# Performance work log

Hardware: AMD Instinct MI355X
Metric: run time of the kernel (lower is better)

The kernel has to match this reference:

```python
import jax, jax.numpy as jnp
import numpy as np

# Attention(d_model=1024, d_head=64, h=16, fastmax=True) -> fastmax_custom path with
# mask=True, normalize=True, temperature=1, a0=1, a1=1, lim=1, p=1, zero RPE.
B, N, D_MODEL, H, D_HEAD = 1, 2048, 1024, 16, 64
A0, A1, LIM = 1.0, 1.0, 1.0


def setup_inputs() -> dict:
    key = jax.random.key(0)
    ks = jax.random.split(key, 6)
    s = 1.0 / np.sqrt(D_MODEL).astype(np.float32)
    return {
        "X": jax.random.normal(ks[0], (B, N, D_MODEL), jnp.float32),
        "Wq": jax.random.normal(ks[1], (H * D_HEAD, D_MODEL), jnp.float32) * s,
        "Wk": jax.random.normal(ks[2], (H * D_HEAD, D_MODEL), jnp.float32) * s,
        "Wv": jax.random.normal(ks[3], (H * D_HEAD, D_MODEL), jnp.float32) * s,
        "Wo": jax.random.normal(ks[4], (D_MODEL, H * D_HEAD), jnp.float32) * s,
        "bo": jnp.zeros((D_MODEL,), jnp.float32),
    }


def _fastmax_causal_p1(q, k, v):
    # q,k,v: [b,h,n,d]. fastmax normalize: scale q,k so the max per-token L2 norm
    # (over the sequence, per batch-head) equals LIM; temperature forced to 1.
    qn = jnp.max(jnp.linalg.norm(q, axis=-1), axis=-1)[..., None, None]  # [b,h,1,1]
    kn = jnp.max(jnp.linalg.norm(k, axis=-1), axis=-1)[..., None, None]
    q = LIM * q / qn
    k = LIM * k / kn
    n = q.shape[2]
    # first-order (p=1) polynomial kernel attention, causal via prefix sums:
    #   score(i,j) = a0 + a1 * <q_i, k_j>,  j <= i
    kv = jnp.cumsum(k[..., :, None] * v[..., None, :], axis=2)  # [b,h,n,d,d]
    num = A0 * jnp.cumsum(v, axis=2) + A1 * jnp.einsum('bhnd,bhnde->bhne', q, kv)
    ksum = jnp.cumsum(k, axis=2)  # [b,h,n,d]
    den = A0 * jnp.arange(1, n + 1, dtype=q.dtype) + A1 * jnp.einsum('bhnd,bhnd->bhn', q, ksum)
    return num / den[..., None]


def reference(X, Wq, Wk, Wv, Wo, bo):
    b, n, _ = X.shape

    def heads(W):
        # [b,n,d_model] @ [d_model,h*d] -> [b,h,n,d]
        return (X @ W.T).reshape(b, n, H, D_HEAD).transpose(0, 2, 1, 3)

    q, k, v = heads(Wq), heads(Wk), heads(Wv)
    vh = _fastmax_causal_p1(q, k, v)                       # [b,h,n,d]
    vh = vh.transpose(0, 2, 1, 3).reshape(b, n, H * D_HEAD)
    return vh @ Wo.T + bo                                  # eval mode: dropout is identity
```

## Files before the change

### kernel.cpp

```cpp
#include <hip/hip_runtime.h>

#define N_SEQ 2048
#define NH 16
#define DH 64
#define CHUNK 64
#define NCHUNK 32

typedef float f32x4 __attribute__((ext_vector_type(4)));
typedef __bf16 bf16x8 __attribute__((ext_vector_type(8)));
typedef unsigned short u16x4 __attribute__((ext_vector_type(4)));
typedef unsigned short u16x8 __attribute__((ext_vector_type(8)));

static __device__ inline unsigned short f2b(float x) {
    unsigned int u = __builtin_bit_cast(unsigned int, x);
    unsigned int r = (u + 0x7fffu + ((u >> 16) & 1u)) >> 16;
    return (unsigned short)r;
}
static __device__ inline float b2f(unsigned short b) {
    return __builtin_bit_cast(float, (unsigned int)b << 16);
}
static __device__ inline int sw(int row, int col) {
    return row * 64 + (col ^ ((row & 7) << 3));
}

__global__ __launch_bounds__(256) void cast_all(
    const float* __restrict__ X, const float* __restrict__ Wq, const float* __restrict__ Wk,
    const float* __restrict__ Wv, const float* __restrict__ Wo,
    unsigned short* __restrict__ Xb, unsigned short* __restrict__ Wb,
    unsigned short* __restrict__ Wob) {
    int i = blockIdx.x * 256 + threadIdx.x;
    const float* src; unsigned short* dst; int off;
    if (i < 524288)       { src = X;  dst = Xb;               off = i; }
    else if (i < 786432)  { src = Wq; dst = Wb;               off = i - 524288; }
    else if (i < 1048576) { src = Wk; dst = Wb + (1u << 20);  off = i - 786432; }
    else if (i < 1310720) { src = Wv; dst = Wb + (2u << 20);  off = i - 1048576; }
    else                  { src = Wo; dst = Wob;              off = i - 1310720; }
    float4 v = reinterpret_cast<const float4*>(src)[off];
    u16x4 o;
    o[0] = f2b(v.x); o[1] = f2b(v.y); o[2] = f2b(v.z); o[3] = f2b(v.w);
    reinterpret_cast<u16x4*>(dst)[off] = o;
}

static __device__ inline void gload_lds16(const unsigned short* g, unsigned short* l) {
    __builtin_amdgcn_global_load_lds(
        (const __attribute__((address_space(1))) unsigned int*)g,
        (__attribute__((address_space(3))) unsigned int*)l, 16, 0, 0);
}

template<int MODE, int BM>
__global__ __launch_bounds__(256, 2) void gemm_bf16(
    const unsigned short* __restrict__ A,
    const unsigned short* __restrict__ B,
    float* __restrict__ outf,
    unsigned short* __restrict__ outb,
    const float* __restrict__ bias,
    int M, int N, int K)
{
    __shared__ __align__(16) unsigned short As[BM][32];
    __shared__ __align__(16) unsigned short Bs[128][32];

    const int L = blockIdx.y * gridDim.x + blockIdx.x;
    const int cpx = (gridDim.x * gridDim.y) >> 3;
    const int tile = (L & 7) * cpx + (L >> 3);
    const int bn = tile / gridDim.y;
    const int bm = tile % gridDim.y;

    const int t = threadIdx.x;
    const int wave = t >> 6, lane = t & 63;
    const int wm = wave >> 1, wn = wave & 1;
    const int r16 = lane & 15, ks = lane >> 4;
    constexpr int MFRAG = BM / 32;

    f32x4 acc[MFRAG][4] = {};

    const unsigned short* gA = A + (size_t)bm * BM * K;
    const unsigned short* gB = B + (size_t)bn * 128 * K;
    const int lrow = lane >> 2;
    const int lcol = (lane & 3) * 8;

    for (int k0 = 0; k0 < K; k0 += 32) {
        __syncthreads();
        #pragma unroll
        for (int p = 0; p < BM / 64; ++p) {
            int row = p * 64 + wave * 16;
            gload_lds16(&gA[(size_t)(row + lrow) * K + k0 + lcol], &As[row][0]);
        }
        #pragma unroll
        for (int p = 0; p < 2; ++p) {
            int row = p * 64 + wave * 16;
            gload_lds16(&gB[(size_t)(row + lrow) * K + k0 + lcol], &Bs[row][0]);
        }
        __syncthreads();

        bf16x8 af[MFRAG], bfr[4];
        #pragma unroll
        for (int m = 0; m < MFRAG; ++m)
            af[m] = *reinterpret_cast<const bf16x8*>(&As[wm * (BM / 2) + m * 16 + r16][ks * 8]);
        #pragma unroll
        for (int n = 0; n < 4; ++n)
            bfr[n] = *reinterpret_cast<const bf16x8*>(&Bs[wn * 64 + n * 16 + r16][ks * 8]);
        #pragma unroll
        for (int m = 0; m < MFRAG; ++m)
            #pragma unroll
            for (int n = 0; n < 4; ++n)
                acc[m][n] = __builtin_amdgcn_mfma_f32_16x16x32_bf16(af[m], bfr[n], acc[m][n], 0, 0, 0);
    }

    #pragma unroll
    for (int m = 0; m < MFRAG; ++m) {
        int row0 = bm * BM + wm * (BM / 2) + m * 16 + ks * 4;
        #pragma unroll
        for (int n = 0; n < 4; ++n) {
            int col = bn * 128 + wn * 64 + n * 16 + r16;
            if (MODE == 0) {
                int wch = col >> 10, h = (col >> 6) & 15, d = col & 63;
                unsigned short* dst = outb + (size_t)wch * (NH * (size_t)N_SEQ * DH)
                                          + (size_t)h * N_SEQ * DH + d;
                #pragma unroll
                for (int j = 0; j < 4; ++j)
                    dst[(size_t)(row0 + j) * DH] = f2b(acc[m][n][j]);
            } else {
                float bv = bias[col];
                #pragma unroll
                for (int j = 0; j < 4; ++j)
                    outf[(size_t)(row0 + j) * N + col] = acc[m][n][j] + bv;
            }
        }
    }
}

__global__ __launch_bounds__(256) void norms1(const unsigned short* __restrict__ QK,
                                              float* __restrict__ partial) {
    const int b = blockIdx.x;
    const int rc = b & 7, h = (b >> 3) & 15, which = b >> 7;
    const int t = threadIdx.x;
    const unsigned short* base = QK + ((size_t)(which * 16 + h) * N_SEQ + rc * 256 + t) * DH;
    float s = 0.f;
    #pragma unroll
    for (int i = 0; i < 8; ++i) {
        u16x8 v = *reinterpret_cast<const u16x8*>(base + i * 8);
        #pragma unroll
        for (int j = 0; j < 8; ++j) { float f = b2f(v[j]); s += f * f; }
    }
    #pragma unroll
    for (int off = 1; off < 64; off <<= 1) s = fmaxf(s, __shfl_xor(s, off));
    __shared__ float red[4];
    if ((t & 63) == 0) red[t >> 6] = s;
    __syncthreads();
    if (t == 0) partial[b] = fmaxf(fmaxf(red[0], red[1]), fmaxf(red[2], red[3]));
}

__global__ __launch_bounds__(256) void chunk_sums(const unsigned short* __restrict__ Kb,
                                                  const unsigned short* __restrict__ Vb,
                                                  unsigned short* __restrict__ Ssum,
                                                  float* __restrict__ zsum,
                                                  float* __restrict__ vssum) {
    const int h = blockIdx.x >> 5, c = blockIdx.x & 31;
    __shared__ __align__(16) unsigned short Kt[4096];
    __shared__ __align__(16) unsigned short Vt[4096];
    const size_t off = ((size_t)h * N_SEQ + c * CHUNK) * DH;
    const int t = threadIdx.x, lane = t & 63;

    {
        const int d = t & 63, j0 = (t >> 6) * 16;
        unsigned short rk[16], rv[16];
        #pragma unroll
        for (int i = 0; i < 16; ++i) {
            rk[i] = Kb[off + (size_t)(j0 + i) * DH + d];
            rv[i] = Vb[off + (size_t)(j0 + i) * DH + d];
        }
        u16x8 a, b;
        #pragma unroll
        for (int i = 0; i < 8; ++i) { a[i] = rk[i]; b[i] = rk[8 + i]; }
        *reinterpret_cast<u16x8*>(&Kt[sw(d, j0)]) = a;
        *reinterpret_cast<u16x8*>(&Kt[sw(d, j0 + 8)]) = b;
        #pragma unroll
        for (int i = 0; i < 8; ++i) { a[i] = rv[i]; b[i] = rv[8 + i]; }
        *reinterpret_cast<u16x8*>(&Vt[sw(d, j0)]) = a;
        *reinterpret_cast<u16x8*>(&Vt[sw(d, j0 + 8)]) = b;
    }
    __syncthreads();

    const int w = t >> 6, cl = lane & 15, g = lane >> 4;
    bf16x8 ak0 = *reinterpret_cast<const bf16x8*>(&Kt[sw(w * 16 + cl, g * 8)]);
    bf16x8 ak1 = *reinterpret_cast<const bf16x8*>(&Kt[sw(w * 16 + cl, 32 + g * 8)]);
    f32x4 acc[4] = {};
    #pragma unroll
    for (int et = 0; et < 4; ++et) {
        bf16x8 b0 = *reinterpret_cast<const bf16x8*>(&Vt[sw(et * 16 + cl, g * 8)]);
        bf16x8 b1 = *reinterpret_cast<const bf16x8*>(&Vt[sw(et * 16 + cl, 32 + g * 8)]);
        acc[et] = __builtin_amdgcn_mfma_f32_16x16x32_bf16(ak0, b0, acc[et], 0, 0, 0);
        acc[et] = __builtin_amdgcn_mfma_f32_16x16x32_bf16(ak1, b1, acc[et], 0, 0, 0);
    }
    unsigned short* So = Ssum + (size_t)blockIdx.x * (DH * DH);
    #pragma unroll
    for (int et = 0; et < 4; ++et)
        #pragma unroll
        for (int j = 0; j < 4; ++j)
            So[(size_t)(w * 16 + g * 4 + j) * DH + et * 16 + cl] = f2b(acc[et][j]);

    if (t < 64) {
        float z = 0.f;
        #pragma unroll
        for (int i = 0; i < 8; ++i) {
            u16x8 v = *reinterpret_cast<const u16x8*>(&Kt[sw(t, i * 8)]);
            #pragma unroll
            for (int k = 0; k < 8; ++k) z += b2f(v[k]);
        }
        zsum[(size_t)blockIdx.x * DH + t] = z;
    } else if (t < 128) {
        int e = t - 64;
        float z = 0.f;
        #pragma unroll
        for (int i = 0; i < 8; ++i) {
            u16x8 v = *reinterpret_cast<const u16x8*>(&Vt[sw(e, i * 8)]);
            #pragma unroll
            for (int k = 0; k < 8; ++k) z += b2f(v[k]);
        }
        vssum[(size_t)blockIdx.x * DH + e] = z;
    }
}

__global__ __launch_bounds__(256) void chunk_scan(unsigned short* __restrict__ Ssum,
                                                  float* __restrict__ zsum,
                                                  float* __restrict__ vssum) {
    const int b = blockIdx.x;
    if (b < 256) {
        const int h = b >> 4;
        const int e = (b & 15) * 256 + threadIdx.x;
        size_t base = (size_t)h * NCHUNK * (DH * DH) + e;
        float run = 0.f;
        for (int c = 0; c < NCHUNK; ++c) {
            size_t idx = base + (size_t)c * (DH * DH);
            float tmp = b2f(Ssum[idx]); Ssum[idx] = f2b(run); run += tmp;
        }
    } else {
        const int g = (b - 256) * 256 + threadIdx.x;
        const int which = g >> 10, h = (g >> 6) & 15, e = g & 63;
        float* arr = which ? vssum : zsum;
        size_t base = (size_t)h * NCHUNK * DH + e;
        float run = 0.f;
        for (int c = 0; c < NCHUNK; ++c) {
            size_t idx = base + (size_t)c * DH;
            float tmp = arr[idx]; arr[idx] = run; run += tmp;
        }
    }
}

__global__ __launch_bounds__(256) void intra_attn(
    const unsigned short* __restrict__ Qb, const unsigned short* __restrict__ Kb,
    const unsigned short* __restrict__ Vb,
    const unsigned short* __restrict__ Ssum, const float* __restrict__ zsum,
    const float* __restrict__ vssum, const float* __restrict__ partial,
    unsigned short* __restrict__ vhb) {
    const int h = blockIdx.x >> 5, c = blockIdx.x & 31;
    __shared__ __align__(16) unsigned short Ql[4096];
    __shared__ __align__(16) unsigned short Kl[4096];
    __shared__ __align__(16) unsigned short Vt[4096];
    __shared__ __align__(16) unsigned short Sp[4096];
    __shared__ __align__(16) unsigned short Pl[4096];
    __shared__ float zp[DH], vsp[DH];

    const int t = threadIdx.x, lane = t & 63, w = t >> 6;
    float qm = 0.f, km = 0.f;
    #pragma unroll
    for (int j2 = 0; j2 < 8; ++j2) {
        qm = fmaxf(qm, partial[h * 8 + j2]);
        km = fmaxf(km, partial[128 + h * 8 + j2]);
    }
    const float alpha = 1.f / sqrtf(qm * km);
    const size_t off = ((size_t)h * N_SEQ + c * CHUNK) * DH;

    #pragma unroll
    for (int p = 0; p < 2; ++p) {
        int lin = t + p * 256;
        int row = lin >> 3, col = (lin & 7) * 8;
        u16x8 q = *reinterpret_cast<const u16x8*>(Qb + off + (size_t)row * DH + col);
        u16x8 k = *reinterpret_cast<const u16x8*>(Kb + off + (size_t)row * DH + col);
        *reinterpret_cast<u16x8*>(&Ql[sw(row, col)]) = q;
        *reinterpret_cast<u16x8*>(&Kl[sw(row, col)]) = k;
    }
    {
        const int e = t & 63, j0 = (t >> 6) * 16;
        unsigned short rv[16];
        #pragma unroll
        for (int i = 0; i < 16; ++i) rv[i] = Vb[off + (size_t)(j0 + i) * DH + e];
        u16x8 a, b;
        #pragma unroll
        for (int i = 0; i < 8; ++i) { a[i] = rv[i]; b[i] = rv[8 + i]; }
        *reinterpret_cast<u16x8*>(&Vt[sw(e, j0)]) = a;
        *reinterpret_cast<u16x8*>(&Vt[sw(e, j0 + 8)]) = b;
    }
    {
        const unsigned short* Sg = Ssum + (size_t)blockIdx.x * (DH * DH);
        const int e = t & 63, d0 = (t >> 6) * 16;
        u16x8 a, b;
        #pragma unroll
        for (int i = 0; i < 8; ++i) a[i] = f2b(alpha * b2f(Sg[(size_t)(d0 + i) * DH + e]));
        #pragma unroll
        for (int i = 0; i < 8; ++i) b[i] = f2b(alpha * b2f(Sg[(size_t)(d0 + 8 + i) * DH + e]));
        *reinterpret_cast<u16x8*>(&Sp[sw(e, d0)]) = a;
        *reinterpret_cast<u16x8*>(&Sp[sw(e, d0 + 8)]) = b;
    }
    if (t < 64) zp[t] = alpha * zsum[(size_t)blockIdx.x * DH + t];
    else if (t < 128) vsp[t - 64] = vssum[(size_t)blockIdx.x * DH + (t - 64)];
    __syncthreads();

    const int cl = lane & 15, g = lane >> 4;
    const int qrow = (w << 4) + cl;

    bf16x8 aq0 = *reinterpret_cast<const bf16x8*>(&Ql[sw(qrow, g * 8)]);
    bf16x8 aq1 = *reinterpret_cast<const bf16x8*>(&Ql[sw(qrow, 32 + g * 8)]);

    f32x4 acc[4] = {};
    #pragma unroll
    for (int et = 0; et < 4; ++et) {
        bf16x8 b0 = *reinterpret_cast<const bf16x8*>(&Sp[sw(et * 16 + cl, g * 8)]);
        bf16x8 b1 = *reinterpret_cast<const bf16x8*>(&Sp[sw(et * 16 + cl, 32 + g * 8)]);
        acc[et] = __builtin_amdgcn_mfma_f32_16x16x32_bf16(aq0, b0, acc[et], 0, 0, 0);
        acc[et] = __builtin_amdgcn_mfma_f32_16x16x32_bf16(aq1, b1, acc[et], 0, 0, 0);
    }
    f32x4 sacc[4] = {};
    #pragma unroll
    for (int kt = 0; kt < 4; ++kt) {
        bf16x8 b0 = *reinterpret_cast<const bf16x8*>(&Kl[sw(kt * 16 + cl, g * 8)]);
        bf16x8 b1 = *reinterpret_cast<const bf16x8*>(&Kl[sw(kt * 16 + cl, 32 + g * 8)]);
        sacc[kt] = __builtin_amdgcn_mfma_f32_16x16x32_bf16(aq0, b0, sacc[kt], 0, 0, 0);
        sacc[kt] = __builtin_amdgcn_mfma_f32_16x16x32_bf16(aq1, b1, sacc[kt], 0, 0, 0);
    }
    unsigned short* Pw = &Pl[w * 1024];
    float part[4] = {0.f, 0.f, 0.f, 0.f};
    #pragma unroll
    for (int kt = 0; kt < 4; ++kt) {
        int key = kt * 16 + cl;
        #pragma unroll
        for (int j = 0; j < 4; ++j) {
            int rr = g * 4 + j;
            int q = (w << 4) + rr;
            float s = (key <= q) ? fmaf(alpha, sacc[kt][j], 1.f) : 0.f;
            part[j] += s;
            Pw[rr * 64 + (key ^ ((rr & 7) << 3))] = f2b(s);
        }
    }
    #pragma unroll
    for (int j = 0; j < 4; ++j) {
        int q = (w << 4) + g * 4 + j;
        float qz = 0.f;
        #pragma unroll
        for (int m = 0; m < 4; ++m) {
            int d = cl + m * 16;
            qz = fmaf(b2f(Ql[sw(q, d)]), zp[d], qz);
        }
        part[j] += qz;
    }
    #pragma unroll
    for (int o = 1; o < 16; o <<= 1)
        #pragma unroll
        for (int j = 0; j < 4; ++j) part[j] += __shfl_xor(part[j], o);
    float invden[4];
    #pragma unroll
    for (int j = 0; j < 4; ++j) invden[j] = 1.f / ((float)(c * CHUNK) + part[j]);

    #pragma unroll
    for (int ks = 0; ks < 2; ++ks) {
        bf16x8 ap = *reinterpret_cast<const bf16x8*>(&Pw[cl * 64 + ((ks * 32 + g * 8) ^ ((cl & 7) << 3))]);
        #pragma unroll
        for (int et = 0; et < 4; ++et) {
            bf16x8 bv = *reinterpret_cast<const bf16x8*>(&Vt[sw(et * 16 + cl, ks * 32 + g * 8)]);
            acc[et] = __builtin_amdgcn_mfma_f32_16x16x32_bf16(ap, bv, acc[et], 0, 0, 0);
        }
    }
    #pragma unroll
    for (int et = 0; et < 4; ++et)
        #pragma unroll
        for (int j = 0; j < 4; ++j) {
            int q = (w << 4) + g * 4 + j;
            int e = et * 16 + cl;
            float o = (vsp[e] + acc[et][j]) * invden[j];
            vhb[(size_t)(c * CHUNK + q) * (NH * DH) + h * DH + e] = f2b(o);
        }
}

extern "C" void kernel_launch(void* const* d_in, const int* in_sizes, int n_in,
                              void* d_out, int out_size, void* d_ws, size_t ws_size,
                              hipStream_t stream) {
    const float* X  = (const float*)d_in[0];
    const float* Wq = (const float*)d_in[1];
    const float* Wk = (const float*)d_in[2];
    const float* Wv = (const float*)d_in[3];
    const float* Wo = (const float*)d_in[4];
    const float* bo = (const float*)d_in[5];
    float* out = (float*)d_out;

    char* w = (char*)d_ws;
    unsigned short* Xb   = (unsigned short*)(w);
    unsigned short* Wb   = (unsigned short*)(w + (4u  << 20));
    unsigned short* Wob  = (unsigned short*)(w + (10u << 20));
    unsigned short* Qb   = (unsigned short*)(w + (12u << 20));
    unsigned short* vhb  = (unsigned short*)(w + (24u << 20));
    float*          partial = (float*)(w + (28u << 20));
    unsigned short* Ssum = (unsigned short*)(w + (29u << 20));
    float*          zsum = (float*)(w + (34u << 20));
    float*          vssum= (float*)(w + (34u << 20) + (1u << 17));
    unsigned short* Kb = Qb + 2097152;
    unsigned short* Vb = Qb + 2u * 2097152;

    cast_all<<<6144, 256, 0, stream>>>(X, Wq, Wk, Wv, Wo, Xb, Wb, Wob);
    gemm_bf16<0, 128><<<dim3(24, 16), 256, 0, stream>>>(Xb, Wb, nullptr, Qb, nullptr, 2048, 3072, 1024);
    norms1<<<256, 256, 0, stream>>>(Qb, partial);
    chunk_sums<<<512, 256, 0, stream>>>(Kb, Vb, Ssum, zsum, vssum);
    chunk_scan<<<264, 256, 0, stream>>>(Ssum, zsum, vssum);
    intra_attn<<<512, 256, 0, stream>>>(Qb, Kb, Vb, Ssum, zsum, vssum, partial, vhb);
    gemm_bf16<1, 64><<<dim3(8, 32), 256, 0, stream>>>(vhb, Wob, out, nullptr, bo, 2048, 1024, 1024);
}
```

Before: 72.08 us.

## Fuse Q/K norm max into QKV GEMM epilogue and double GEMM K-tile

The separate norms1 kernel is removed. The QKV GEMM epilogue now computes per-row squared L2 norms from fp32 accumulators and reduces them into a per-head max with atomicMax, using a buffer zeroed in cast_all. The GEMM K step also grows from 32 to 64 with an XOR-swizzled LDS layout, halving loop iterations and barriers at the cost of more LDS per block. Norms now come from fp32 accumulators rather than bf16-rounded values, which slightly changes numerics, and the atomicMax on float bits relies on the values being non-negative.

```diff
diff --git a/kernel.cpp b/kernel.cpp
--- a/kernel.cpp
+++ b/kernel.cpp
@@ -27,7 +27,8 @@
     const float* __restrict__ X, const float* __restrict__ Wq, const float* __restrict__ Wk,
     const float* __restrict__ Wv, const float* __restrict__ Wo,
     unsigned short* __restrict__ Xb, unsigned short* __restrict__ Wb,
-    unsigned short* __restrict__ Wob) {
+    unsigned short* __restrict__ Wob, float* __restrict__ nrm) {
+    if (blockIdx.x == 0 && threadIdx.x < 32) nrm[threadIdx.x] = 0.f;
     int i = blockIdx.x * 256 + threadIdx.x;
     const float* src; unsigned short* dst; int off;
     if (i < 524288)       { src = X;  dst = Xb;               off = i; }
@@ -54,10 +55,11 @@
     float* __restrict__ outf,
     unsigned short* __restrict__ outb,
     const float* __restrict__ bias,
+    float* __restrict__ nrm,
     int M, int N, int K)
 {
-    __shared__ __align__(16) unsigned short As[BM][32];
-    __shared__ __align__(16) unsigned short Bs[128][32];
+    __shared__ __align__(16) unsigned short As[BM][64];
+    __shared__ __align__(16) unsigned short Bs[128][64];
 
     const int L = blockIdx.y * gridDim.x + blockIdx.x;
     const int cpx = (gridDim.x * gridDim.y) >> 3;
@@ -75,35 +77,40 @@
 
     const unsigned short* gA = A + (size_t)bm * BM * K;
     const unsigned short* gB = B + (size_t)bn * 128 * K;
-    const int lrow = lane >> 2;
-    const int lcol = (lane & 3) * 8;
-
-    for (int k0 = 0; k0 < K; k0 += 32) {
+    const int lrow = lane >> 3;
+    const int scol = (((lane & 7) ^ (lrow & 7)) << 3);
+    const int rsw = (r16 & 7) << 3;
+
+    for (int k0 = 0; k0 < K; k0 += 64) {
         __syncthreads();
         #pragma unroll
-        for (int p = 0; p < BM / 64; ++p) {
-            int row = p * 64 + wave * 16;
-            gload_lds16(&gA[(size_t)(row + lrow) * K + k0 + lcol], &As[row][0]);
-        }
-        #pragma unroll
-        for (int p = 0; p < 2; ++p) {
-            int row = p * 64 + wave * 16;
-            gload_lds16(&gB[(size_t)(row + lrow) * K + k0 + lcol], &Bs[row][0]);
+        for (int g = 0; g < BM / 32; ++g) {
+            int r0 = wave * (BM / 4) + g * 8;
+            gload_lds16(&gA[(size_t)(r0 + lrow) * K + k0 + scol], &As[r0][0]);
+        }
+        #pragma unroll
+        for (int g = 0; g < 4; ++g) {
+            int r0 = wave * 32 + g * 8;
+            gload_lds16(&gB[(size_t)(r0 + lrow) * K + k0 + scol], &Bs[r0][0]);
         }
         __syncthreads();
 
-        bf16x8 af[MFRAG], bfr[4];
-        #pragma unroll
-        for (int m = 0; m < MFRAG; ++m)
-            af[m] = *reinterpret_cast<const bf16x8*>(&As[wm * (BM / 2) + m * 16 + r16][ks * 8]);
-        #pragma unroll
-        for (int n = 0; n < 4; ++n)
-            bfr[n] = *reinterpret_cast<const bf16x8*>(&Bs[wn * 64 + n * 16 + r16][ks * 8]);
-        #pragma unroll
-        for (int m = 0; m < MFRAG; ++m)
+        #pragma unroll
+        for (int ksub = 0; ksub < 2; ++ksub) {
+            const int sl = (((ksub << 2) + ks) << 3) ^ rsw;
+            bf16x8 af[MFRAG], bfr[4];
+            #pragma unroll
+            for (int m = 0; m < MFRAG; ++m)
+                af[m] = *reinterpret_cast<const bf16x8*>(&As[wm * (BM / 2) + m * 16 + r16][sl]);
             #pragma unroll
             for (int n = 0; n < 4; ++n)
-                acc[m][n] = __builtin_amdgcn_mfma_f32_16x16x32_bf16(af[m], bfr[n], acc[m][n], 0, 0, 0);
+                bfr[n] = *reinterpret_cast<const bf16x8*>(&Bs[wn * 64 + n * 16 + r16][sl]);
+            #pragma unroll
+            for (int m = 0; m < MFRAG; ++m)
+                #pragma unroll
+                for (int n = 0; n < 4; ++n)
+                    acc[m][n] = __builtin_amdgcn_mfma_f32_16x16x32_bf16(af[m], bfr[n], acc[m][n], 0, 0, 0);
+        }
     }
 
     #pragma unroll
@@ -127,27 +134,33 @@
             }
         }
     }
-}
-
-__global__ __launch_bounds__(256) void norms1(const unsigned short* __restrict__ QK,
-                                              float* __restrict__ partial) {
-    const int b = blockIdx.x;
-    const int rc = b & 7, h = (b >> 3) & 15, which = b >> 7;
-    const int t = threadIdx.x;
-    const unsigned short* base = QK + ((size_t)(which * 16 + h) * N_SEQ + rc * 256 + t) * DH;
-    float s = 0.f;
-    #pragma unroll
-    for (int i = 0; i < 8; ++i) {
-        u16x8 v = *reinterpret_cast<const u16x8*>(base + i * 8);
-        #pragma unroll
-        for (int j = 0; j < 8; ++j) { float f = b2f(v[j]); s += f * f; }
-    }
-    #pragma unroll
-    for (int off = 1; off < 64; off <<= 1) s = fmaxf(s, __shfl_xor(s, off));
-    __shared__ float red[4];
-    if ((t & 63) == 0) red[t >> 6] = s;
-    __syncthreads();
-    if (t == 0) partial[b] = fmaxf(fmaxf(red[0], red[1]), fmaxf(red[2], red[3]));
+
+    if (MODE == 0) {
+        const int colbase = bn * 128 + wn * 64;
+        const int wch = colbase >> 10;
+        if (wch < 2) {
+            const int h = (colbase >> 6) & 15;
+            float mx = 0.f;
+            #pragma unroll
+            for (int m = 0; m < MFRAG; ++m)
+                #pragma unroll
+                for (int j = 0; j < 4; ++j) {
+                    float rs = 0.f;
+                    #pragma unroll
+                    for (int n = 0; n < 4; ++n) rs = fmaf(acc[m][n][j], acc[m][n][j], rs);
+                    rs += __shfl_xor(rs, 1);
+                    rs += __shfl_xor(rs, 2);
+                    rs += __shfl_xor(rs, 4);
+                    rs += __shfl_xor(rs, 8);
+                    mx = fmaxf(mx, rs);
+                }
+            mx = fmaxf(mx, __shfl_xor(mx, 16));
+            mx = fmaxf(mx, __shfl_xor(mx, 32));
+            if (lane == 0)
+                atomicMax(reinterpret_cast<unsigned int*>(&nrm[wch * 16 + h]),
+                          __builtin_bit_cast(unsigned int, mx));
+        }
+    }
 }
 
 __global__ __launch_bounds__(256) void chunk_sums(const unsigned short* __restrict__ Kb,
@@ -251,7 +264,7 @@
     const unsigned short* __restrict__ Qb, const unsigned short* __restrict__ Kb,
     const unsigned short* __restrict__ Vb,
     const unsigned short* __restrict__ Ssum, const float* __restrict__ zsum,
-    const float* __restrict__ vssum, const float* __restrict__ partial,
+    const float* __restrict__ vssum, const float* __restrict__ nrm,
     unsigned short* __restrict__ vhb) {
     const int h = blockIdx.x >> 5, c = blockIdx.x & 31;
     __shared__ __align__(16) unsigned short Ql[4096];
@@ -262,13 +275,7 @@
     __shared__ float zp[DH], vsp[DH];
 
     const int t = threadIdx.x, lane = t & 63, w = t >> 6;
-    float qm = 0.f, km = 0.f;
-    #pragma unroll
-    for (int j2 = 0; j2 < 8; ++j2) {
-        qm = fmaxf(qm, partial[h * 8 + j2]);
-        km = fmaxf(km, partial[128 + h * 8 + j2]);
-    }
-    const float alpha = 1.f / sqrtf(qm * km);
+    const float alpha = 1.f / sqrtf(nrm[h] * nrm[16 + h]);
     const size_t off = ((size_t)h * N_SEQ + c * CHUNK) * DH;
 
     #pragma unroll
@@ -398,18 +405,17 @@
     unsigned short* Wob  = (unsigned short*)(w + (10u << 20));
     unsigned short* Qb   = (unsigned short*)(w + (12u << 20));
     unsigned short* vhb  = (unsigned short*)(w + (24u << 20));
-    float*          partial = (float*)(w + (28u << 20));
+    float*          nrm  = (float*)(w + (28u << 20));
     unsigned short* Ssum = (unsigned short*)(w + (29u << 20));
     float*          zsum = (float*)(w + (34u << 20));
     float*          vssum= (float*)(w + (34u << 20) + (1u << 17));
     unsigned short* Kb = Qb + 2097152;
     unsigned short* Vb = Qb + 2u * 2097152;
 
-    cast_all<<<6144, 256, 0, stream>>>(X, Wq, Wk, Wv, Wo, Xb, Wb, Wob);
-    gemm_bf16<0, 128><<<dim3(24, 16), 256, 0, stream>>>(Xb, Wb, nullptr, Qb, nullptr, 2048, 3072, 1024);
-    norms1<<<256, 256, 0, stream>>>(Qb, partial);
+    cast_all<<<6144, 256, 0, stream>>>(X, Wq, Wk, Wv, Wo, Xb, Wb, Wob, nrm);
+    gemm_bf16<0, 128><<<dim3(24, 16), 256, 0, stream>>>(Xb, Wb, nullptr, Qb, nullptr, nrm, 2048, 3072, 1024);
     chunk_sums<<<512, 256, 0, stream>>>(Kb, Vb, Ssum, zsum, vssum);
     chunk_scan<<<264, 256, 0, stream>>>(Ssum, zsum, vssum);
-    intra_attn<<<512, 256, 0, stream>>>(Qb, Kb, Vb, Ssum, zsum, vssum, partial, vhb);
-    gemm_bf16<1, 64><<<dim3(8, 32), 256, 0, stream>>>(vhb, Wob, out, nullptr, bo, 2048, 1024, 1024);
-}
+    intra_attn<<<512, 256, 0, stream>>>(Qb, Kb, Vb, Ssum, zsum, vssum, nrm, vhb);
+    gemm_bf16<1, 64><<<dim3(8, 32), 256, 0, stream>>>(vhb, Wob, out, nullptr, bo, nullptr, 2048, 1024, 1024);
+}
```

Result: faster. 68.50 us (-5.0%).
